# Kernel optimization log

Measured on AMD Instinct MI355X. Metric: run time of the kernel, lower is better.

The kernel has to match this reference:

```python
import jax, jax.numpy as jnp
import numpy as np

EPS = 1e-5

def layer_norm(x, w, b):
    m = jnp.mean(x, axis=-1, keepdims=True)
    v = jnp.mean(jnp.square(x - m), axis=-1, keepdims=True)
    return (x - m) * jax.lax.rsqrt(v + EPS) * w + b

def time_shift(x):
    # shift sequence right by one, zero-pad first step: (B,L,D)
    return jnp.pad(x[:, :-1], ((0, 0), (1, 0), (0, 0)))

def wkv(time_decay, time_first, k, v):
    # Numerically-stable RWKV v4 WKV recurrence. k,v: (B,L,D)
    w = -jnp.exp(time_decay)  # (D,) negative decay
    u = time_first            # (D,)
    B, L, D = k.shape
    kT = jnp.swapaxes(k, 0, 1)  # (L,B,D)
    vT = jnp.swapaxes(v, 0, 1)
    a0 = jnp.zeros((B, D), k.dtype)
    b0 = jnp.zeros((B, D), k.dtype)
    p0 = jnp.full((B, D), -1e38, k.dtype)

    def step(carry, kv_t):
        a, b, p = carry
        k_t, v_t = kv_t
        ww = u + k_t
        q = jnp.maximum(p, ww)
        e1 = jnp.exp(p - q)
        e2 = jnp.exp(ww - q)
        out = (e1 * a + e2 * v_t) / (e1 * b + e2)
        ww2 = p + w
        q2 = jnp.maximum(ww2, k_t)
        e1b = jnp.exp(ww2 - q2)
        e2b = jnp.exp(k_t - q2)
        return (e1b * a + e2b * v_t, e1b * b + e2b, q2), out

    _, outs = jax.lax.scan(step, (a0, b0, p0), (kT, vT))
    return jnp.swapaxes(outs, 0, 1)  # (B,L,D)

def setup_inputs() -> dict:
    key = jax.random.key(0)
    B, L, D, D_att, D_ffn = 8, 2048, 1024, 1024, 4096
    ks = jax.random.split(key, 16)
    s = 1.0 / np.sqrt(D)
    inp = {
        "x": jax.random.normal(ks[0], (B, L, D), jnp.float32),
        "ln_att_w": jnp.ones((D,), jnp.float32),
        "ln_att_b": jnp.zeros((D,), jnp.float32),
        "ln_ffn_w": jnp.ones((D,), jnp.float32),
        "ln_ffn_b": jnp.zeros((D,), jnp.float32),
        "att_time_decay": jax.random.normal(ks[1], (D_att,), jnp.float32) * 0.5,
        "att_time_first": jax.random.normal(ks[2], (D_att,), jnp.float32) * 0.5,
        "att_mix_k": jax.random.uniform(ks[3], (D,), jnp.float32),
        "att_mix_v": jax.random.uniform(ks[4], (D,), jnp.float32),
        "att_mix_r": jax.random.uniform(ks[5], (D,), jnp.float32),
        "att_Wk": jax.random.normal(ks[6], (D_att, D), jnp.float32) * s,
        "att_Wv": jax.random.normal(ks[7], (D_att, D), jnp.float32) * s,
        "att_Wr": jax.random.normal(ks[8], (D_att, D), jnp.float32) * s,
        "att_Wo": jax.random.normal(ks[9], (D, D_att), jnp.float32) * s,
        "ffn_mix_k": jax.random.uniform(ks[10], (D,), jnp.float32),
        "ffn_mix_r": jax.random.uniform(ks[11], (D,), jnp.float32),
        "ffn_Wk": jax.random.normal(ks[12], (D_ffn, D), jnp.float32) * s,
        "ffn_Wv": jax.random.normal(ks[13], (D, D_ffn), jnp.float32) * (1.0 / np.sqrt(D_ffn)),
        "ffn_Wr": jax.random.normal(ks[14], (D, D), jnp.float32) * s,
    }
    return inp

def rwkv_block(x, ln_att_w, ln_att_b, ln_ffn_w, ln_ffn_b,
               att_time_decay, att_time_first, att_mix_k, att_mix_v, att_mix_r,
               att_Wk, att_Wv, att_Wr, att_Wo,
               ffn_mix_k, ffn_mix_r, ffn_Wk, ffn_Wv, ffn_Wr):
    # --- time-mix (WKV attention) ---
    xa = layer_norm(x, ln_att_w, ln_att_b)
    xs = time_shift(xa)
    k = jnp.einsum('bld,ad->bla', xa * att_mix_k + xs * (1.0 - att_mix_k), att_Wk)
    v = jnp.einsum('bld,ad->bla', xa * att_mix_v + xs * (1.0 - att_mix_v), att_Wv)
    r = jnp.einsum('bld,ad->bla', xa * att_mix_r + xs * (1.0 - att_mix_r), att_Wr)
    att = jnp.einsum('bla,da->bld', jax.nn.sigmoid(r) * wkv(att_time_decay, att_time_first, k, v), att_Wo)
    x = x + att
    # --- channel-mix FFN ---
    xf = layer_norm(x, ln_ffn_w, ln_ffn_b)
    xs = time_shift(xf)
    kx = xf * ffn_mix_k + xs * (1.0 - ffn_mix_k)
    rx = xf * ffn_mix_r + xs * (1.0 - ffn_mix_r)
    h = jnp.square(jax.nn.relu(jnp.einsum('bld,fd->blf', kx, ffn_Wk)))
    ffn = jax.nn.sigmoid(jnp.einsum('bld,ed->ble', rx, ffn_Wr)) * jnp.einsum('blf,df->bld', h, ffn_Wv)
    return x + ffn

def reference(x, ln_att_w, ln_att_b, ln_ffn_w, ln_ffn_b,
              att_time_decay, att_time_first, att_mix_k, att_mix_v, att_mix_r,
              att_Wk, att_Wv, att_Wr, att_Wo,
              ffn_mix_k, ffn_mix_r, ffn_Wk, ffn_Wv, ffn_Wr):
    return rwkv_block(x, ln_att_w, ln_att_b, ln_ffn_w, ln_ffn_b,
                      att_time_decay, att_time_first, att_mix_k, att_mix_v, att_mix_r,
                      att_Wk, att_Wv, att_Wr, att_Wo,
                      ffn_mix_k, ffn_mix_r, ffn_Wk, ffn_Wv, ffn_Wr)
```

## Files before the change

kernel.cpp:

```cpp
#include <hip/hip_runtime.h>
#include <stdint.h>

#define DDIM 1024
#define LSEQ 2048
#define BSZ  8
#define FDIM 4096
#define MROWS (BSZ*LSEQ)
#define NCHUNK 32
#define CLEN  (LSEQ/NCHUNK)

typedef float        f32x4  __attribute__((ext_vector_type(4)));
typedef unsigned int u32x4  __attribute__((ext_vector_type(4)));
typedef short        short8 __attribute__((ext_vector_type(8)));

using gas_void = const __attribute__((address_space(1))) void;
using las_void = __attribute__((address_space(3))) void;

__device__ __forceinline__ void gload16(const void* g, void* l) {
    __builtin_amdgcn_global_load_lds((gas_void*)g, (las_void*)l, 16, 0, 0);
}

__device__ __forceinline__ f32x4 mfma16(short8 a, short8 b, f32x4 c) {
    return __builtin_amdgcn_mfma_f32_16x16x32_bf16(a, b, c, 0, 0, 0);
}

__device__ __forceinline__ unsigned short f2bf(float f) {
    __bf16 h = (__bf16)f;
    return __builtin_bit_cast(unsigned short, h);
}

struct CvtArgs {
    const float* s[7];
    __bf16*      d[7];
    int          cum[8];
};

__global__ __launch_bounds__(256) void cvt_all(CvtArgs a)
{
    const int i = blockIdx.x * 256 + threadIdx.x;
    if (i >= a.cum[7]) return;
    int seg = 0;
#pragma unroll 6
    while (i >= a.cum[seg + 1]) ++seg;
    const int off = i - a.cum[seg];
    float4 f = ((const float4*)a.s[seg])[off];
    ushort4 o;
    o.x = f2bf(f.x); o.y = f2bf(f.y); o.z = f2bf(f.z); o.w = f2bf(f.w);
    ((ushort4*)a.d[seg])[off] = o;
}

__device__ __forceinline__ void blk_reduce4(float& a, float& b, float& c, float& d) {
#pragma unroll
    for (int off = 32; off >= 1; off >>= 1) {
        a += __shfl_xor(a, off, 64);
        b += __shfl_xor(b, off, 64);
        c += __shfl_xor(c, off, 64);
        d += __shfl_xor(d, off, 64);
    }
    __shared__ float sm[4][4];
    const int tid = threadIdx.x;
    if ((tid & 63) == 0) {
        sm[tid >> 6][0] = a; sm[tid >> 6][1] = b;
        sm[tid >> 6][2] = c; sm[tid >> 6][3] = d;
    }
    __syncthreads();
    a = sm[0][0] + sm[1][0] + sm[2][0] + sm[3][0];
    b = sm[0][1] + sm[1][1] + sm[2][1] + sm[3][1];
    c = sm[0][2] + sm[1][2] + sm[2][2] + sm[3][2];
    d = sm[0][3] + sm[1][3] + sm[2][3] + sm[3][3];
}

__global__ __launch_bounds__(256) void ln_mix3(
    const float* __restrict__ xin, const float* __restrict__ lnw, const float* __restrict__ lnb,
    const float* __restrict__ mkv, const float* __restrict__ mvv, const float* __restrict__ mrv,
    __bf16* __restrict__ ok, __bf16* __restrict__ ov, __bf16* __restrict__ orr)
{
    const int row = blockIdx.x;
    const int l   = row & (LSEQ - 1);
    const int tid = threadIdx.x;
    const size_t rbase = (size_t)row * DDIM;
    const float4 cur = ((const float4*)(xin + rbase))[tid];
    float4 prv = make_float4(0.f, 0.f, 0.f, 0.f);
    if (l > 0) prv = ((const float4*)(xin + rbase - DDIM))[tid];
    float s0 = cur.x + cur.y + cur.z + cur.w;
    float q0 = cur.x*cur.x + cur.y*cur.y + cur.z*cur.z + cur.w*cur.w;
    float s1 = prv.x + prv.y + prv.z + prv.w;
    float q1 = prv.x*prv.x + prv.y*prv.y + prv.z*prv.z + prv.w*prv.w;
    blk_reduce4(s0, q0, s1, q1);
    const float inv = 1.f / (float)DDIM;
    const float m0 = s0 * inv, m1 = s1 * inv;
    const float r0 = rsqrtf(fmaxf(q0 * inv - m0*m0, 0.f) + 1e-5f);
    const float r1 = rsqrtf(fmaxf(q1 * inv - m1*m1, 0.f) + 1e-5f);
    const float4 w4 = ((const float4*)lnw)[tid];
    const float4 b4 = ((const float4*)lnb)[tid];
    const float4 k4 = ((const float4*)mkv)[tid];
    const float4 v4 = ((const float4*)mvv)[tid];
    const float4 r4 = ((const float4*)mrv)[tid];
    const float cA[4] = {cur.x, cur.y, cur.z, cur.w};
    const float pA[4] = {prv.x, prv.y, prv.z, prv.w};
    const float wA[4] = {w4.x, w4.y, w4.z, w4.w};
    const float bA[4] = {b4.x, b4.y, b4.z, b4.w};
    const float kA[4] = {k4.x, k4.y, k4.z, k4.w};
    const float vA[4] = {v4.x, v4.y, v4.z, v4.w};
    const float rA[4] = {r4.x, r4.y, r4.z, r4.w};
    ushort4 pk, pv, pr;
    unsigned short* pkp = &pk.x; unsigned short* pvp = &pv.x; unsigned short* prp = &pr.x;
#pragma unroll
    for (int j = 0; j < 4; ++j) {
        float xa = (cA[j] - m0) * r0 * wA[j] + bA[j];
        float xs = (l > 0) ? ((pA[j] - m1) * r1 * wA[j] + bA[j]) : 0.f;
        pkp[j] = f2bf(xa * kA[j] + xs * (1.f - kA[j]));
        pvp[j] = f2bf(xa * vA[j] + xs * (1.f - vA[j]));
        prp[j] = f2bf(xa * rA[j] + xs * (1.f - rA[j]));
    }
    const size_t oi = (size_t)row * (DDIM/4) + tid;
    ((ushort4*)ok)[oi]  = pk;
    ((ushort4*)ov)[oi]  = pv;
    ((ushort4*)orr)[oi] = pr;
}

__global__ __launch_bounds__(256) void ln_mix2(
    const float* __restrict__ xin, const float* __restrict__ lnw, const float* __restrict__ lnb,
    const float* __restrict__ mkv, const float* __restrict__ mrv,
    __bf16* __restrict__ ok, __bf16* __restrict__ orr)
{
    const int row = blockIdx.x;
    const int l   = row & (LSEQ - 1);
    const int tid = threadIdx.x;
    const size_t rbase = (size_t)row * DDIM;
    const float4 cur = ((const float4*)(xin + rbase))[tid];
    float4 prv = make_float4(0.f, 0.f, 0.f, 0.f);
    if (l > 0) prv = ((const float4*)(xin + rbase - DDIM))[tid];
    float s0 = cur.x + cur.y + cur.z + cur.w;
    float q0 = cur.x*cur.x + cur.y*cur.y + cur.z*cur.z + cur.w*cur.w;
    float s1 = prv.x + prv.y + prv.z + prv.w;
    float q1 = prv.x*prv.x + prv.y*prv.y + prv.z*prv.z + prv.w*prv.w;
    blk_reduce4(s0, q0, s1, q1);
    const float inv = 1.f / (float)DDIM;
    const float m0 = s0 * inv, m1 = s1 * inv;
    const float r0 = rsqrtf(fmaxf(q0 * inv - m0*m0, 0.f) + 1e-5f);
    const float r1 = rsqrtf(fmaxf(q1 * inv - m1*m1, 0.f) + 1e-5f);
    const float4 w4 = ((const float4*)lnw)[tid];
    const float4 b4 = ((const float4*)lnb)[tid];
    const float4 k4 = ((const float4*)mkv)[tid];
    const float4 r4 = ((const float4*)mrv)[tid];
    const float cA[4] = {cur.x, cur.y, cur.z, cur.w};
    const float pA[4] = {prv.x, prv.y, prv.z, prv.w};
    const float wA[4] = {w4.x, w4.y, w4.z, w4.w};
    const float bA[4] = {b4.x, b4.y, b4.z, b4.w};
    const float kA[4] = {k4.x, k4.y, k4.z, k4.w};
    const float rA[4] = {r4.x, r4.y, r4.z, r4.w};
    ushort4 pk, pr;
    unsigned short* pkp = &pk.x; unsigned short* prp = &pr.x;
#pragma unroll
    for (int j = 0; j < 4; ++j) {
        float xa = (cA[j] - m0) * r0 * wA[j] + bA[j];
        float xs = (l > 0) ? ((pA[j] - m1) * r1 * wA[j] + bA[j]) : 0.f;
        pkp[j] = f2bf(xa * kA[j] + xs * (1.f - kA[j]));
        prp[j] = f2bf(xa * rA[j] + xs * (1.f - rA[j]));
    }
    const size_t oi = (size_t)row * (DDIM/4) + tid;
    ((ushort4*)ok)[oi]  = pk;
    ((ushort4*)orr)[oi] = pr;
}

__global__ __launch_bounds__(256) void wkv_phase1(
    const __bf16* __restrict__ kin, const __bf16* __restrict__ vin,
    const float* __restrict__ td,
    float* __restrict__ sa, float* __restrict__ sb, float* __restrict__ sp)
{
    const int idx = blockIdx.x * 256 + threadIdx.x;
    const int d  = idx & (DDIM - 1);
    const int bc = idx >> 10;
    const int b  = bc & (BSZ - 1);
    const int c  = bc >> 3;
    const float w = -__expf(td[d]);
    const size_t base = ((size_t)b * LSEQ + (size_t)c * CLEN) * DDIM + d;
    float a = 0.f, bbv = 0.f, p = -1e38f;
    for (int t = 0; t < CLEN; ++t) {
        const size_t off = base + (size_t)t * DDIM;
        const float kt = (float)kin[off];
        const float vt = (float)vin[off];
        const float ww2 = p + w;
        const float q2  = fmaxf(ww2, kt);
        const float e1  = __expf(ww2 - q2);
        const float e2  = __expf(kt - q2);
        a   = e1 * a   + e2 * vt;
        bbv = e1 * bbv + e2;
        p   = q2;
    }
    sa[idx] = a; sb[idx] = bbv; sp[idx] = p;
}

__global__ __launch_bounds__(256) void wkv_phase2(
    const __bf16* __restrict__ kin, const __bf16* __restrict__ vin,
    const __bf16* __restrict__ srin,
    const float* __restrict__ td, const float* __restrict__ tf,
    const float* __restrict__ sa, const float* __restrict__ sb,
    const float* __restrict__ sp,
    __bf16* __restrict__ outp)
{
    const int idx = blockIdx.x * 256 + threadIdx.x;
    const int d  = idx & (DDIM - 1);
    const int bc = idx >> 10;
    const int b  = bc & (BSZ - 1);
    const int c  = bc >> 3;
    const float w = -__expf(td[d]);
    const float u = tf[d];
    const float nw = (float)CLEN * w;

    float a = 0.f, bbv = 0.f, p = -1e38f;
    for (int j = 0; j < c; ++j) {
        const int sidx = ((j * BSZ + b) << 10) + d;
        const float aj = sa[sidx], bj = sb[sidx], pj = sp[sidx];
        const float ps = p + nw;
        const float pn = fmaxf(ps, pj);
        const float e1 = __expf(ps - pn);
        const float e2 = __expf(pj - pn);
        a   = e1 * a   + e2 * aj;
        bbv = e1 * bbv + e2 * bj;
        p   = pn;
    }

    const size_t base = ((size_t)b * LSEQ + (size_t)c * CLEN) * DDIM + d;
    for (int t = 0; t < CLEN; ++t) {
        const size_t off = base + (size_t)t * DDIM;
        const float kt = (float)kin[off];
        const float vt = (float)vin[off];
        const float sr = (float)srin[off];
        const float ww = u + kt;
        const float q  = fmaxf(p, ww);
        const float e1 = __expf(p - q);
        const float e2 = __expf(ww - q);
        const float o  = (e1 * a + e2 * vt) / (e1 * bbv + e2);
        outp[off] = (__bf16)(sr * o);
        const float ww2 = p + w;
        const float q2  = fmaxf(ww2, kt);
        const float e1b = __expf(ww2 - q2);
        const float e2b = __expf(kt - q2);
        a   = e1b * a   + e2b * vt;
        bbv = e1b * bbv + e2b;
        p   = q2;
    }
}

template<int EPI>
__global__ __launch_bounds__(512, 2)
void gemm8(const __bf16* __restrict__ A, const __bf16* __restrict__ Bw,
           float* outF, __bf16* outH,
           const float* auxF, const __bf16* __restrict__ auxH,
           int N, int K, int gy)
{
    __shared__ __align__(16) char smem[131072];
    const int tid  = threadIdx.x;
    const int lane = tid & 63;
    const int wid  = tid >> 6;
    const int wr = wid >> 2, wc = wid & 3;

    const int nwg = gridDim.x;
    const int f = blockIdx.x;
    const int g = (f & 7) * (nwg >> 3) + (f >> 3);
    const int tx = g / gy;
    const int ty = g - tx * gy;
    const size_t row0 = (size_t)tx * 256;
    const size_t col0 = (size_t)ty * 256;

    const int nt = K >> 6;
    const int iters = K >> 7;

    auto stage_half = [&](int d, int X, int kh, int ktile) {
        const int kc = (ktile < nt ? ktile : nt - 1);
        const int kg = kc * 64 + kh * 32;
#pragma unroll
        for (int q = 0; q < 2; ++q) {
            const int row   = q * 128 + wid * 16 + (lane >> 2);
            const int chunk = (lane & 3) ^ ((row >> 1) & 3);
            const __bf16* gp = (X ? Bw + (col0 + row) * (size_t)K
                                  : A  + (row0 + row) * (size_t)K) + kg + chunk * 8;
            char* lp = smem + d * 65536 + X * 32768 + kh * 16384 + q * 8192 + wid * 1024;
            gload16(gp, lp);
        }
    };
    auto rdA = [&](int d, int ks, int m) -> short8 {
        const int row  = wr * 128 + m * 16 + (lane & 15);
        const int slot = (lane >> 4) ^ ((row >> 1) & 3);
        return *(const short8*)(smem + d * 65536 + ks * 16384 + row * 64 + slot * 16);
    };
    auto rdB = [&](int d, int ks, int n) -> short8 {
        const int row  = wc * 64 + n * 16 + (lane & 15);
        const int slot = (lane >> 4) ^ ((row >> 1) & 3);
        return *(const short8*)(smem + d * 65536 + 32768 + ks * 16384 + row * 64 + slot * 16);
    };

    f32x4 acc[8][4] = {};
    short8 bfr[4];

#define VM6 asm volatile("s_waitcnt vmcnt(6)" ::: "memory")

#define PHASE(d, ks, mh, RD8, STAGE_STMT, VMW)                                   \
    {                                                                            \
        short8 afr[4];                                                           \
        _Pragma("unroll")                                                        \
        for (int m = 0; m < 4; ++m) afr[m] = rdA(d, ks, (mh) * 4 + m);           \
        if (RD8) {                                                               \
            _Pragma("unroll")                                                    \
            for (int n = 0; n < 4; ++n) bfr[n] = rdB(d, ks, n);                  \
        }                                                                        \
        STAGE_STMT;                                                              \
        VMW;                                                                     \
        __builtin_amdgcn_s_barrier();                                            \
        __builtin_amdgcn_s_setprio(1);                                           \
        _Pragma("unroll")                                                        \
        for (int m = 0; m < 4; ++m) {                                            \
            _Pragma("unroll")                                                    \
            for (int n = 0; n < 4; ++n)                                          \
                acc[(mh) * 4 + m][n] = mfma16(afr[m], bfr[n], acc[(mh) * 4 + m][n]); \
        }                                                                        \
        __builtin_amdgcn_s_setprio(0);                                           \
        __builtin_amdgcn_s_barrier();                                            \
    }

    stage_half(0, 0, 0, 0); stage_half(0, 0, 1, 0);
    stage_half(0, 1, 0, 0); stage_half(0, 1, 1, 0);
    stage_half(1, 1, 0, 1); stage_half(1, 0, 0, 1); stage_half(1, 1, 1, 1);
    VM6;
    __builtin_amdgcn_s_barrier();

    for (int it = 0; it < iters; ++it) {
        const int kt = 2 * it;
        PHASE(0, 0, 0, 1, stage_half(1, 0, 1, kt + 1), );
        PHASE(0, 0, 1, 0, stage_half(0, 1, 0, kt + 2), );
        PHASE(0, 1, 0, 1, stage_half(0, 0, 0, kt + 2), );
        PHASE(0, 1, 1, 0, stage_half(0, 1, 1, kt + 2), VM6);
        PHASE(1, 0, 0, 1, stage_half(0, 0, 1, kt + 2), );
        PHASE(1, 0, 1, 0, stage_half(1, 1, 0, kt + 3), );
        PHASE(1, 1, 0, 1, stage_half(1, 0, 0, kt + 3), );
        PHASE(1, 1, 1, 0, stage_half(1, 1, 1, kt + 3), VM6);
    }
#undef PHASE
#undef VM6

    const size_t obr = row0 + wr * 128 + ((lane >> 4) << 2);
    const size_t obc = col0 + wc * 64 + (lane & 15);
#pragma unroll
    for (int m = 0; m < 8; ++m) {
#pragma unroll
        for (int n = 0; n < 4; ++n) {
#pragma unroll
            for (int j = 0; j < 4; ++j) {
                const size_t idx = (obr + m * 16 + j) * (size_t)N + obc + n * 16;
                const float v = acc[m][n][j];
                if constexpr (EPI == 1) {
                    outH[idx] = (__bf16)(1.f / (1.f + __expf(-v)));
                } else if constexpr (EPI == 2) {
                    const float t2 = fmaxf(v, 0.f);
                    outH[idx] = (__bf16)(t2 * t2);
                } else if constexpr (EPI == 3) {
                    outF[idx] = auxF[idx] + v;
                } else if constexpr (EPI == 4) {
                    outF[idx] = auxF[idx] + (float)auxH[idx] * v;
                } else {
                    outH[idx] = (__bf16)v;
                }
            }
        }
    }
}

extern "C" void kernel_launch(void* const* d_in, const int* in_sizes, int n_in,
                              void* d_out, int out_size, void* d_ws, size_t ws_size,
                              hipStream_t stream)
{
    const float* x    = (const float*)d_in[0];
    const float* lnaw = (const float*)d_in[1];
    const float* lnab = (const float*)d_in[2];
    const float* lnfw = (const float*)d_in[3];
    const float* lnfb = (const float*)d_in[4];
    const float* tdec = (const float*)d_in[5];
    const float* tfir = (const float*)d_in[6];
    const float* amk  = (const float*)d_in[7];
    const float* amv  = (const float*)d_in[8];
    const float* amr  = (const float*)d_in[9];
    const float* aWk  = (const float*)d_in[10];
    const float* aWv  = (const float*)d_in[11];
    const float* aWr  = (const float*)d_in[12];
    const float* aWo  = (const float*)d_in[13];
    const float* fmk  = (const float*)d_in[14];
    const float* fmr  = (const float*)d_in[15];
    const float* fWk  = (const float*)d_in[16];
    const float* fWv  = (const float*)d_in[17];
    const float* fWr  = (const float*)d_in[18];
    float* out = (float*)d_out;

    char* ws = (char*)d_ws;
    const size_t MiB = 1ull << 20;
    __bf16* Wk_h  = (__bf16*)ws;
    __bf16* Wv_h  = Wk_h + (1ull << 20);
    __bf16* Wr_h  = Wk_h + (2ull << 20);
    __bf16* Wo_h  = Wk_h + (3ull << 20);
    __bf16* fWk_h = Wk_h + (4ull << 20);
    __bf16* fWv_h = Wk_h + (8ull << 20);
    __bf16* fWr_h = Wk_h + (12ull << 20);
    __bf16* xk = (__bf16*)(ws + 26 * MiB);
    __bf16* xv = (__bf16*)(ws + 58 * MiB);
    __bf16* xr = (__bf16*)(ws + 90 * MiB);
    __bf16* kb = (__bf16*)(ws + 122 * MiB);
    __bf16* vb = (__bf16*)(ws + 154 * MiB);
    __bf16* sr = (__bf16*)(ws + 186 * MiB);
    float* st_a = (float*)(ws + 218 * MiB);
    float* st_b = (float*)(ws + 219 * MiB);
    float* st_p = (float*)(ws + 220 * MiB);
    __bf16* atta = xk;
    __bf16* kx   = xv;
    __bf16* rx   = xr;
    __bf16* sb   = xk;
    __bf16* hb   = (__bf16*)(ws + 90 * MiB);

    CvtArgs ca;
    ca.s[0] = aWk;  ca.d[0] = Wk_h;
    ca.s[1] = aWv;  ca.d[1] = Wv_h;
    ca.s[2] = aWr;  ca.d[2] = Wr_h;
    ca.s[3] = aWo;  ca.d[3] = Wo_h;
    ca.s[4] = fWk;  ca.d[4] = fWk_h;
    ca.s[5] = fWv;  ca.d[5] = fWv_h;
    ca.s[6] = fWr;  ca.d[6] = fWr_h;
    {
        const int sz[7] = {1<<18, 1<<18, 1<<18, 1<<18, 1<<20, 1<<20, 1<<18};
        int c = 0;
        for (int i = 0; i < 7; ++i) { ca.cum[i] = c; c += sz[i]; }
        ca.cum[7] = c;
    }
    cvt_all<<<(ca.cum[7] + 255) / 256, 256, 0, stream>>>(ca);

    ln_mix3<<<MROWS, 256, 0, stream>>>(x, lnaw, lnab, amk, amv, amr, xk, xv, xr);

    const int gD = (MROWS / 256) * (DDIM / 256);
    const int gF = (MROWS / 256) * (FDIM / 256);
    gemm8<5><<<gD, 512, 0, stream>>>(xk, Wk_h, nullptr, kb, nullptr, nullptr, DDIM, DDIM, DDIM/256);
    gemm8<5><<<gD, 512, 0, stream>>>(xv, Wv_h, nullptr, vb, nullptr, nullptr, DDIM, DDIM, DDIM/256);
    gemm8<1><<<gD, 512, 0, stream>>>(xr, Wr_h, nullptr, sr, nullptr, nullptr, DDIM, DDIM, DDIM/256);

    const int nthreads = BSZ * DDIM * NCHUNK;
    wkv_phase1<<<nthreads / 256, 256, 0, stream>>>(kb, vb, tdec, st_a, st_b, st_p);
    wkv_phase2<<<nthreads / 256, 256, 0, stream>>>(kb, vb, sr, tdec, tfir,
                                                   st_a, st_b, st_p, atta);

    gemm8<3><<<gD, 512, 0, stream>>>(atta, Wo_h, out, nullptr, x, nullptr, DDIM, DDIM, DDIM/256);

    ln_mix2<<<MROWS, 256, 0, stream>>>(out, lnfw, lnfb, fmk, fmr, kx, rx);

    gemm8<1><<<gD, 512, 0, stream>>>(rx, fWr_h, nullptr, sb, nullptr, nullptr, DDIM, DDIM, DDIM/256);

    gemm8<2><<<gF, 512, 0, stream>>>(kx, fWk_h, nullptr, hb, nullptr, nullptr, FDIM, DDIM, FDIM/256);

    gemm8<4><<<gD, 512, 0, stream>>>(hb, fWv_h, out, nullptr, out, sb, DDIM, FDIM, DDIM/256);
}
```

Measured before the change: 723.6 us.

## Batch K/V/R projection GEMMs into one launch and restructure barrier placement

Merges the three attention-input projection GEMMs into a single 768-workgroup launch. Each 256-block slab selects its A, B and output buffer by pointer offset, which assumes xk/xv/xr, the weights and kb/vb/sr are laid out contiguously. The per-phase double barrier becomes one barrier at the start of each phase, and the vmcnt waits move accordingly. This aims to cut launch overhead and tail underutilization and to reduce synchronization per K-step. It risks LDS races from removing the trailing barrier, and relies on the workspace layout matching the offsets.

```diff
diff --git a/kernel.cpp b/kernel.cpp
--- a/kernel.cpp
+++ b/kernel.cpp
@@ -10,7 +10,6 @@
 #define CLEN  (LSEQ/NCHUNK)
 
 typedef float        f32x4  __attribute__((ext_vector_type(4)));
-typedef unsigned int u32x4  __attribute__((ext_vector_type(4)));
 typedef short        short8 __attribute__((ext_vector_type(8)));
 
 using gas_void = const __attribute__((address_space(1))) void;
@@ -257,8 +256,17 @@
     const int wid  = tid >> 6;
     const int wr = wid >> 2, wc = wid & 3;
 
-    const int nwg = gridDim.x;
-    const int f = blockIdx.x;
+    int f = blockIdx.x;
+    int nwg = gridDim.x;
+    bool sig = false;
+    if constexpr (EPI == 7) {
+        const int slab = f >> 8;
+        f &= 255; nwg = 256;
+        A    += (size_t)slab * (16u << 20);
+        Bw   += (size_t)slab << 20;
+        outH += (size_t)slab << 24;
+        sig = (slab == 2);
+    }
     const int g = (f & 7) * (nwg >> 3) + (f >> 3);
     const int tx = g / gy;
     const int ty = g - tx * gy;
@@ -299,6 +307,8 @@
 
 #define PHASE(d, ks, mh, RD8, STAGE_STMT, VMW)                                   \
     {                                                                            \
+        VMW;                                                                     \
+        __builtin_amdgcn_s_barrier();                                            \
         short8 afr[4];                                                           \
         _Pragma("unroll")                                                        \
         for (int m = 0; m < 4; ++m) afr[m] = rdA(d, ks, (mh) * 4 + m);           \
@@ -307,8 +317,6 @@
             for (int n = 0; n < 4; ++n) bfr[n] = rdB(d, ks, n);                  \
         }                                                                        \
         STAGE_STMT;                                                              \
-        VMW;                                                                     \
-        __builtin_amdgcn_s_barrier();                                            \
         __builtin_amdgcn_s_setprio(1);                                           \
         _Pragma("unroll")                                                        \
         for (int m = 0; m < 4; ++m) {                                            \
@@ -317,25 +325,22 @@
                 acc[(mh) * 4 + m][n] = mfma16(afr[m], bfr[n], acc[(mh) * 4 + m][n]); \
         }                                                                        \
         __builtin_amdgcn_s_setprio(0);                                           \
-        __builtin_amdgcn_s_barrier();                                            \
     }
 
     stage_half(0, 0, 0, 0); stage_half(0, 0, 1, 0);
     stage_half(0, 1, 0, 0); stage_half(0, 1, 1, 0);
     stage_half(1, 1, 0, 1); stage_half(1, 0, 0, 1); stage_half(1, 1, 1, 1);
-    VM6;
-    __builtin_amdgcn_s_barrier();
 
     for (int it = 0; it < iters; ++it) {
         const int kt = 2 * it;
-        PHASE(0, 0, 0, 1, stage_half(1, 0, 1, kt + 1), );
+        PHASE(0, 0, 0, 1, stage_half(1, 0, 1, kt + 1), VM6);
         PHASE(0, 0, 1, 0, stage_half(0, 1, 0, kt + 2), );
         PHASE(0, 1, 0, 1, stage_half(0, 0, 0, kt + 2), );
-        PHASE(0, 1, 1, 0, stage_half(0, 1, 1, kt + 2), VM6);
-        PHASE(1, 0, 0, 1, stage_half(0, 0, 1, kt + 2), );
+        PHASE(0, 1, 1, 0, stage_half(0, 1, 1, kt + 2), );
+        PHASE(1, 0, 0, 1, stage_half(0, 0, 1, kt + 2), VM6);
         PHASE(1, 0, 1, 0, stage_half(1, 1, 0, kt + 3), );
         PHASE(1, 1, 0, 1, stage_half(1, 0, 0, kt + 3), );
-        PHASE(1, 1, 1, 0, stage_half(1, 1, 1, kt + 3), VM6);
+        PHASE(1, 1, 1, 0, stage_half(1, 1, 1, kt + 3), );
     }
 #undef PHASE
 #undef VM6
@@ -359,6 +364,8 @@
                     outF[idx] = auxF[idx] + v;
                 } else if constexpr (EPI == 4) {
                     outF[idx] = auxF[idx] + (float)auxH[idx] * v;
+                } else if constexpr (EPI == 7) {
+                    outH[idx] = (__bf16)(sig ? (1.f / (1.f + __expf(-v))) : v);
                 } else {
                     outH[idx] = (__bf16)v;
                 }
@@ -434,24 +441,20 @@
 
     ln_mix3<<<MROWS, 256, 0, stream>>>(x, lnaw, lnab, amk, amv, amr, xk, xv, xr);
 
-    const int gD = (MROWS / 256) * (DDIM / 256);
-    const int gF = (MROWS / 256) * (FDIM / 256);
-    gemm8<5><<<gD, 512, 0, stream>>>(xk, Wk_h, nullptr, kb, nullptr, nullptr, DDIM, DDIM, DDIM/256);
-    gemm8<5><<<gD, 512, 0, stream>>>(xv, Wv_h, nullptr, vb, nullptr, nullptr, DDIM, DDIM, DDIM/256);
-    gemm8<1><<<gD, 512, 0, stream>>>(xr, Wr_h, nullptr, sr, nullptr, nullptr, DDIM, DDIM, DDIM/256);
+    gemm8<7><<<768, 512, 0, stream>>>(xk, Wk_h, nullptr, kb, nullptr, nullptr, DDIM, DDIM, DDIM/256);
 
     const int nthreads = BSZ * DDIM * NCHUNK;
     wkv_phase1<<<nthreads / 256, 256, 0, stream>>>(kb, vb, tdec, st_a, st_b, st_p);
     wkv_phase2<<<nthreads / 256, 256, 0, stream>>>(kb, vb, sr, tdec, tfir,
                                                    st_a, st_b, st_p, atta);
 
-    gemm8<3><<<gD, 512, 0, stream>>>(atta, Wo_h, out, nullptr, x, nullptr, DDIM, DDIM, DDIM/256);
+    gemm8<3><<<256, 512, 0, stream>>>(atta, Wo_h, out, nullptr, x, nullptr, DDIM, DDIM, DDIM/256);
 
     ln_mix2<<<MROWS, 256, 0, stream>>>(out, lnfw, lnfb, fmk, fmr, kx, rx);
 
-    gemm8<1><<<gD, 512, 0, stream>>>(rx, fWr_h, nullptr, sb, nullptr, nullptr, DDIM, DDIM, DDIM/256);
-
-    gemm8<2><<<gF, 512, 0, stream>>>(kx, fWk_h, nullptr, hb, nullptr, nullptr, FDIM, DDIM, FDIM/256);
-
-    gemm8<4><<<gD, 512, 0, stream>>>(hb, fWv_h, out, nullptr, out, sb, DDIM, FDIM, DDIM/256);
-}
+    gemm8<1><<<256, 512, 0, stream>>>(rx, fWr_h, nullptr, sb, nullptr, nullptr, DDIM, DDIM, DDIM/256);
+
+    gemm8<2><<<1024, 512, 0, stream>>>(kx, fWk_h, nullptr, hb, nullptr, nullptr, FDIM, DDIM, FDIM/256);
+
+    gemm8<4><<<256, 512, 0, stream>>>(hb, fWv_h, out, nullptr, out, sb, DDIM, FDIM, DDIM/256);
+}
```

Result: no change. 715.0 us (-1.2%).
